# Optimization experiments

Measured on AMD Instinct MI355X. Metric: run time of the kernel, lower is better.

## Reference

```python
import jax, jax.numpy as jnp
import numpy as np

B, S, E, H = 2, 2048, 1024, 16
D = E // H


def setup_inputs() -> dict:
    key = jax.random.key(0)
    ks = jax.random.split(key, 12)
    init = lambda k, shp: (jax.random.normal(k, shp, dtype=jnp.float32) * 0.02)
    return {
        "q": jax.random.normal(ks[0], (B, S, E), dtype=jnp.float32),
        "k": jax.random.normal(ks[1], (B, S, E), dtype=jnp.float32),
        "v": jax.random.normal(ks[2], (B, S, E), dtype=jnp.float32),
        "wq": init(ks[3], (E, E)), "bq": jnp.zeros((E,), jnp.float32),
        "wk": init(ks[4], (E, E)), "bk": jnp.zeros((E,), jnp.float32),
        "wv": init(ks[5], (E, E)), "bv": jnp.zeros((E,), jnp.float32),
        "wo": init(ks[6], (E, E)), "bo": jnp.zeros((E,), jnp.float32),
        "gamma": jnp.ones((E,), jnp.float32),
        "beta": jnp.zeros((E,), jnp.float32),
        "mask": 1,
    }


def _split_heads(x):
    # [B,S,E] -> [B,H,S,D]
    return x.reshape(x.shape[0], x.shape[1], H, D).transpose(0, 2, 1, 3)


def _mha(q, k, v, wq, bq, wk, bk, wv, bv, wo, bo, gamma, beta, causal):
    residual = q
    query = _split_heads(q @ wq + bq)
    key = _split_heads(k @ wk + bk)
    value = _split_heads(v @ wv + bv)
    scale = jnp.sqrt(jnp.float32(D)) + 1e-8  # matches torch: sqrt(dk) + 1e-8
    score = jnp.einsum("bhqd,bhkd->bhqk", query, key) / scale
    if causal:
        cm = jnp.tril(jnp.ones((S, S), dtype=bool))  # 1 - triu(...,1)
        score = jnp.where(cm[None, None], score, -jnp.inf)
    attn = jax.nn.softmax(score, axis=-1)
    ctx = jnp.einsum("bhqk,bhkd->bhqd", attn, value)
    ctx = ctx.transpose(0, 2, 1, 3).reshape(ctx.shape[0], S, E)
    o = ctx @ wo + bo  # dropout is identity in eval mode
    x = residual + o
    mu = jnp.mean(x, axis=-1, keepdims=True)
    var = jnp.var(x, axis=-1, keepdims=True)
    return (x - mu) / jnp.sqrt(var + 1e-5) * gamma + beta


def reference(q, k, v, wq, bq, wk, bk, wv, bv, wo, bo, gamma, beta, mask):
    return _mha(q, k, v, wq, bq, wk, bk, wv, bv, wo, bo, gamma, beta, bool(mask))
```

## Files before the change

### kernel.cpp

```cpp
#include <hip/hip_runtime.h>
#include <hip/hip_bf16.h>

typedef __bf16 bf16x8 __attribute__((ext_vector_type(8)));
typedef __attribute__((ext_vector_type(8))) short short8_t;
typedef __attribute__((ext_vector_type(4))) short short4_t;
typedef __attribute__((ext_vector_type(4))) float f32x4;

#define DEV __device__ __forceinline__

constexpr int Bc = 2, Sc = 2048, Ec = 1024, Hc = 16, Dc = 64;
constexpr int Mc = Bc * Sc;
constexpr int NT = Sc / 64;
constexpr float kQS = (float)((1.0 / (8.0 + 1e-8)) * 1.4426950408889634);

DEV short f2bf(float f) {
  unsigned int u = __builtin_bit_cast(unsigned int, f);
  unsigned int r = u + 0x7fffu + ((u >> 16) & 1u);
  return (short)(r >> 16);
}
DEV short bfc(float f) { __bf16 h = (__bf16)f; return __builtin_bit_cast(short, h); }

DEV float fexp2(float x) {
#if __has_builtin(__builtin_amdgcn_exp2f)
  return __builtin_amdgcn_exp2f(x);
#else
  float r;
  asm("v_exp_f32 %0, %1" : "=v"(r) : "v"(x));
  return r;
#endif
}

DEV void gload16(const short* g, short* lds) {
  __builtin_amdgcn_global_load_lds((const __attribute__((address_space(1))) void*)g,
                                   (__attribute__((address_space(3))) void*)lds, 16, 0, 0);
}

struct Prep {
  const float* w[4]; short* wt[4];
  const float* x[3]; short* y[3];
};
__global__ __launch_bounds__(256) void k_prep(Prep a) {
  const int bid = blockIdx.x;
  if (bid < 4096) {
    __shared__ float tile[32][33];
    const int z = bid >> 10, bk = (bid >> 5) & 31, bn = bid & 31;
    const float* w = a.w[z];
    short* wt = a.wt[z];
    int tx = threadIdx.x & 31, ty = threadIdx.x >> 5;
#pragma unroll
    for (int i = 0; i < 4; i++)
      tile[ty + i * 8][tx] = w[(size_t)(bk * 32 + ty + i * 8) * Ec + bn * 32 + tx];
    __syncthreads();
#pragma unroll
    for (int i = 0; i < 4; i++)
      wt[(size_t)(bn * 32 + ty + i * 8) * Ec + bk * 32 + tx] = f2bf(tile[tx][ty + i * 8]);
  } else {
    const int idx = bid - 4096;
    const int z = idx >> 11, c = idx & 2047;
    const float* x = a.x[z];
    short* y = a.y[z];
    size_t i = ((size_t)c * 256 + threadIdx.x) * 8;
    float4 v0 = *(const float4*)(x + i);
    float4 v1 = *(const float4*)(x + i + 4);
    short8_t h;
    h[0] = bfc(v0.x); h[1] = bfc(v0.y); h[2] = bfc(v0.z); h[3] = bfc(v0.w);
    h[4] = bfc(v1.x); h[5] = bfc(v1.y); h[6] = bfc(v1.z); h[7] = bfc(v1.w);
    *(short8_t*)(y + i) = h;
  }
}

DEV void gemm_mfma(const short* lA, const short* lB, f32x4 (&acc)[4][4], int lane, int wm, int wn) {
#pragma unroll
  for (int kc = 0; kc < 2; kc++) {
    bf16x8 a[4], b[4];
#pragma unroll
    for (int mf = 0; mf < 4; mf++) {
      int row = wm * 64 + mf * 16 + (lane & 15);
      int ch = (kc * 4 + (lane >> 4)) ^ (row & 7);
      a[mf] = *(const bf16x8*)&lA[row * 64 + (ch << 3)];
    }
#pragma unroll
    for (int nf = 0; nf < 4; nf++) {
      int row = wn * 64 + nf * 16 + (lane & 15);
      int ch = (kc * 4 + (lane >> 4)) ^ (row & 7);
      b[nf] = *(const bf16x8*)&lB[row * 64 + (ch << 3)];
    }
#pragma unroll
    for (int mf = 0; mf < 4; mf++)
#pragma unroll
      for (int nf = 0; nf < 4; nf++)
        acc[mf][nf] = __builtin_amdgcn_mfma_f32_16x16x32_bf16(a[mf], b[nf], acc[mf][nf], 0, 0, 0);
  }
}

struct QKV3 { const short* A[3]; const short* Bt[3]; const float* bias[3]; short* out[3]; };

__global__ __launch_bounds__(256, 2) void k_gemm_qkv(QKV3 args) {
  __shared__ short lA[2][128 * 64];
  __shared__ short lB[2][128 * 64];
  int lin = blockIdx.x + 8 * blockIdx.y + 256 * blockIdx.z;
  lin = (lin & 7) * 96 + (lin >> 3);
  const int bx = lin & 7, by = (lin >> 3) & 31, z = lin >> 8;
  const short* A = args.A[z];
  const short* Bt = args.Bt[z];
  const float* bias = args.bias[z];
  short* out = args.out[z];
  const int t = threadIdx.x;
  const int m0 = by * 128, n0 = bx * 128;
  const int lane = t & 63, wid = t >> 6;
  const int wm = wid >> 1, wn = wid & 1;
  const int rl = lane >> 3, chs = ((lane & 7) ^ rl) << 3;

  f32x4 acc[4][4];
#pragma unroll
  for (int i = 0; i < 4; i++)
#pragma unroll
    for (int j = 0; j < 4; j++) acc[i][j] = {0.f, 0.f, 0.f, 0.f};

  auto stage = [&](int st, int buf) {
    const int k0 = st * 64;
#pragma unroll
    for (int j = 0; j < 4; j++) {
      int r0 = wid * 32 + j * 8;
      gload16(A + (size_t)(m0 + r0 + rl) * Ec + k0 + chs, &lA[buf][r0 * 64]);
      gload16(Bt + (size_t)(n0 + r0 + rl) * Ec + k0 + chs, &lB[buf][r0 * 64]);
    }
  };
  stage(0, 0);
  stage(1, 1);
  for (int s = 0; s < 15; s++) {
    asm volatile("s_waitcnt vmcnt(8)" ::: "memory");
    __builtin_amdgcn_s_barrier();
    gemm_mfma(lA[s & 1], lB[s & 1], acc, lane, wm, wn);
    __builtin_amdgcn_s_barrier();
    if (s + 2 < 16) stage(s + 2, s & 1);
  }
  asm volatile("s_waitcnt vmcnt(0)" ::: "memory");
  __builtin_amdgcn_s_barrier();
  gemm_mfma(lA[1], lB[1], acc, lane, wm, wn);

#pragma unroll
  for (int mf = 0; mf < 4; mf++) {
#pragma unroll
    for (int nf = 0; nf < 4; nf++) {
      int col = n0 + wn * 64 + nf * 16 + (lane & 15);
      float bs = bias[col];
      int row0 = m0 + wm * 64 + mf * 16 + ((lane >> 4) << 2);
      int bh = ((row0 >> 11) << 4) + (col >> 6);
      int d = col & 63;
      size_t bhbase = (size_t)bh * Sc * Dc;
      if (z == 0) {
#pragma unroll
        for (int r = 0; r < 4; r++) {
          int row = row0 + r;
          size_t off = bhbase + (size_t)(row & 2047) * Dc + d;
          out[off] = f2bf((acc[mf][nf][r] + bs) * kQS);
        }
      } else if (z == 1) {
#pragma unroll
        for (int r = 0; r < 4; r++) {
          int sr = (row0 + r) & 2047;
          size_t off = bhbase + (size_t)(sr >> 4) * 1024 + ((d >> 5) * 512) +
                       (((d >> 3) & 3) * 128) + ((sr & 15) * 8) + (d & 7);
          out[off] = f2bf(acc[mf][nf][r] + bs);
        }
      } else {
        short4_t h;
#pragma unroll
        for (int r = 0; r < 4; r++) h[r] = f2bf(acc[mf][nf][r] + bs);
        int s0 = row0 & 2047;
        size_t off = bhbase + (size_t)(s0 >> 6) * 4096 + (((s0 >> 5) & 1) * 2048) +
                     (((d >> 4) & 3) * 512) + ((((s0 >> 3) & 3) * 16 + (d & 15)) * 8) + (s0 & 7);
        *(short4_t*)&out[off] = h;
      }
    }
  }
}

__global__ __launch_bounds__(256, 2) void k_gemm_o(const short* __restrict__ A,
                                                   const short* __restrict__ Bt,
                                                   const float* __restrict__ bias,
                                                   const float* __restrict__ res,
                                                   float* __restrict__ out) {
  __shared__ short lA[2][128 * 64];
  __shared__ short lB[2][128 * 64];
  int lin = blockIdx.x + 8 * blockIdx.y;
  lin = (lin & 7) * 32 + (lin >> 3);
  const int bx = lin & 7, by = lin >> 3;
  const int t = threadIdx.x;
  const int m0 = by * 128, n0 = bx * 128;
  const int lane = t & 63, wid = t >> 6;
  const int wm = wid >> 1, wn = wid & 1;
  const int rl = lane >> 3, chs = ((lane & 7) ^ rl) << 3;

  f32x4 acc[4][4];
#pragma unroll
  for (int i = 0; i < 4; i++)
#pragma unroll
    for (int j = 0; j < 4; j++) acc[i][j] = {0.f, 0.f, 0.f, 0.f};

  auto stage = [&](int st, int buf) {
    const int k0 = st * 64;
#pragma unroll
    for (int j = 0; j < 4; j++) {
      int r0 = wid * 32 + j * 8;
      gload16(A + (size_t)(m0 + r0 + rl) * Ec + k0 + chs, &lA[buf][r0 * 64]);
      gload16(Bt + (size_t)(n0 + r0 + rl) * Ec + k0 + chs, &lB[buf][r0 * 64]);
    }
  };
  stage(0, 0);
  stage(1, 1);
  for (int s = 0; s < 15; s++) {
    asm volatile("s_waitcnt vmcnt(8)" ::: "memory");
    __builtin_amdgcn_s_barrier();
    gemm_mfma(lA[s & 1], lB[s & 1], acc, lane, wm, wn);
    __builtin_amdgcn_s_barrier();
    if (s + 2 < 16) stage(s + 2, s & 1);
  }
  asm volatile("s_waitcnt vmcnt(0)" ::: "memory");
  __builtin_amdgcn_s_barrier();
  gemm_mfma(lA[1], lB[1], acc, lane, wm, wn);

#pragma unroll
  for (int mf = 0; mf < 4; mf++) {
#pragma unroll
    for (int nf = 0; nf < 4; nf++) {
      int col = n0 + wn * 64 + nf * 16 + (lane & 15);
      float bs = bias[col];
#pragma unroll
      for (int r = 0; r < 4; r++) {
        int row = m0 + wm * 64 + mf * 16 + ((lane >> 4) << 2) + r;
        out[(size_t)row * Ec + col] = acc[mf][nf][r] + bs + res[(size_t)row * Ec + col];
      }
    }
  }
}

__global__ __launch_bounds__(256, 2) void k_attn8(const short* __restrict__ Qp,
                                                  const short* __restrict__ Kf,
                                                  const short* __restrict__ Vf,
                                                  const int* __restrict__ maskp,
                                                  short* __restrict__ ctx) {
  __shared__ short lP[64 * 64];
  const int lin = blockIdx.x;
  const int bh = lin & 31, qi = lin >> 5;
  const int qtA = qi, qtB = NT - 1 - qi;
  const int t = threadIdx.x, lane = t & 63, w = t >> 6;
  const int gs = lane >> 4, l15 = lane & 15;
  const bool causal = maskp[0] != 0;
  const int b = bh >> 4, h = bh & 15;
  const size_t base = (size_t)bh * Sc * Dc;
  const int ktend = causal ? qtB : (NT - 1);

  bf16x8 aqA[2], aqB[2];
  {
    const short* qpA = Qp + base + (size_t)(qtA * 64 + w * 16 + l15) * Dc + gs * 8;
    const short* qpB = Qp + base + (size_t)(qtB * 64 + w * 16 + l15) * Dc + gs * 8;
    aqA[0] = *(const bf16x8*)(qpA);
    aqA[1] = *(const bf16x8*)(qpA + 32);
    aqB[0] = *(const bf16x8*)(qpB);
    aqB[1] = *(const bf16x8*)(qpB + 32);
  }
  bf16x8 ones;
#pragma unroll
  for (int j = 0; j < 8; j++) ones[j] = (__bf16)1.0f;

  f32x4 oA[4], oB[4], lsA, lsB;
#pragma unroll
  for (int i = 0; i < 4; i++) {
    oA[i] = {0.f, 0.f, 0.f, 0.f};
    oB[i] = {0.f, 0.f, 0.f, 0.f};
  }
  lsA = {0.f, 0.f, 0.f, 0.f};
  lsB = {0.f, 0.f, 0.f, 0.f};

  const int prow = w * 16 + l15, pswz = l15 & 7;
  short* pw[4];
  const short* pr[2];
#pragma unroll
  for (int mf = 0; mf < 4; mf++)
    pw[mf] = &lP[prow * 64 + (((2 * mf + (gs >> 1)) ^ pswz) << 3) + (gs & 1) * 4];
#pragma unroll
  for (int kc = 0; kc < 2; kc++)
    pr[kc] = &lP[prow * 64 + (((kc * 4 + gs) ^ pswz) << 3)];

  const short* Kb = Kf + base + lane * 8;
  const short* Vb = Vf + base + lane * 8;
  const int qloc = w * 16 + l15;

  bf16x8 kA[2][4], kB[2][4];
#pragma unroll
  for (int mf = 0; mf < 4; mf++) {
    kA[0][mf] = *(const bf16x8*)(Kb + mf * 1024);
    kA[1][mf] = *(const bf16x8*)(Kb + mf * 1024 + 512);
  }

  int kt = 0;
  auto tilepass = [&](const bf16x8 (&kc_)[2][4], const bf16x8 (&vf)[2][4],
                      const bf16x8 (&aq)[2], f32x4 (&oacc)[4], f32x4& lsum, bool diag) {
    f32x4 s[4];
#pragma unroll
    for (int mf = 0; mf < 4; mf++) s[mf] = {0.f, 0.f, 0.f, 0.f};
    __builtin_amdgcn_s_setprio(1);
#pragma unroll
    for (int c2 = 0; c2 < 2; c2++)
#pragma unroll
      for (int mf = 0; mf < 4; mf++)
        s[mf] = __builtin_amdgcn_mfma_f32_16x16x32_bf16(kc_[c2][mf], aq[c2], s[mf], 0, 0, 0);
    __builtin_amdgcn_s_setprio(0);
    if (diag) {
#pragma unroll
      for (int mf = 0; mf < 4; mf++) {
        short4_t hh;
#pragma unroll
        for (int r = 0; r < 4; r++) {
          float p = fexp2(s[mf][r]);
          if ((mf * 16 + gs * 4 + r) > qloc) p = 0.f;
          hh[r] = bfc(p);
        }
        *(short4_t*)pw[mf] = hh;
      }
    } else {
#pragma unroll
      for (int mf = 0; mf < 4; mf++) {
        short4_t hh;
#pragma unroll
        for (int r = 0; r < 4; r++) hh[r] = bfc(fexp2(s[mf][r]));
        *(short4_t*)pw[mf] = hh;
      }
    }
    bf16x8 pa[2];
    pa[0] = *(const bf16x8*)pr[0];
    pa[1] = *(const bf16x8*)pr[1];
    __builtin_amdgcn_s_setprio(1);
#pragma unroll
    for (int c2 = 0; c2 < 2; c2++) {
      lsum = __builtin_amdgcn_mfma_f32_16x16x32_bf16(pa[c2], ones, lsum, 0, 0, 0);
#pragma unroll
      for (int df = 0; df < 4; df++)
        oacc[df] = __builtin_amdgcn_mfma_f32_16x16x32_bf16(pa[c2], vf[c2][df], oacc[df], 0, 0, 0);
    }
    __builtin_amdgcn_s_setprio(0);
  };

  auto body = [&](bf16x8 (&kc_)[2][4], bf16x8 (&kn_)[2][4]) {
    if (kt < ktend) {
      const short* kp = Kb + (kt + 1) * 4096;
#pragma unroll
      for (int mf = 0; mf < 4; mf++) {
        kn_[0][mf] = *(const bf16x8*)(kp + mf * 1024);
        kn_[1][mf] = *(const bf16x8*)(kp + mf * 1024 + 512);
      }
    }
    const short* vp = Vb + kt * 4096;
    bf16x8 vf[2][4];
#pragma unroll
    for (int c2 = 0; c2 < 2; c2++)
#pragma unroll
      for (int df = 0; df < 4; df++)
        vf[c2][df] = *(const bf16x8*)(vp + c2 * 2048 + df * 512);
    __builtin_amdgcn_sched_barrier(0);

    tilepass(kc_, vf, aqB, oB, lsB, causal && (kt == qtB));
    if (!causal || (kt <= qtA))
      tilepass(kc_, vf, aqA, oA, lsA, causal && (kt == qtA));
  };

  while (true) {
    body(kA, kB);
    if (++kt > ktend) break;
    body(kB, kA);
    if (++kt > ktend) break;
  }

#pragma unroll
  for (int r = 0; r < 4; r++) {
    float ibB = 1.0f / lsB[r];
    float ibA = 1.0f / lsA[r];
    int srB = qtB * 64 + w * 16 + (gs << 2) + r;
    int srA = qtA * 64 + w * 16 + (gs << 2) + r;
#pragma unroll
    for (int df = 0; df < 4; df++) {
      int col = h * 64 + df * 16 + l15;
      ctx[(size_t)(b * Sc + srB) * Ec + col] = f2bf(oB[df][r] * ibB);
      ctx[(size_t)(b * Sc + srA) * Ec + col] = f2bf(oA[df][r] * ibA);
    }
  }
}

__global__ __launch_bounds__(256) void k_ln(float* __restrict__ x,
                                            const float* __restrict__ gamma,
                                            const float* __restrict__ beta) {
  int row = blockIdx.x, t = threadIdx.x;
  float4 v = *(const float4*)(x + (size_t)row * Ec + t * 4);
  float s = v.x + v.y + v.z + v.w;
  float sq = v.x * v.x + v.y * v.y + v.z * v.z + v.w * v.w;
#pragma unroll
  for (int m = 1; m < 64; m <<= 1) {
    s += __shfl_xor(s, m);
    sq += __shfl_xor(sq, m);
  }
  __shared__ float red[8];
  if ((t & 63) == 0) {
    red[t >> 6] = s;
    red[4 + (t >> 6)] = sq;
  }
  __syncthreads();
  s = red[0] + red[1] + red[2] + red[3];
  sq = red[4] + red[5] + red[6] + red[7];
  float mu = s * (1.f / Ec);
  float var = sq * (1.f / Ec) - mu * mu;
  float rstd = rsqrtf(var + 1e-5f);
  float4 g = *(const float4*)(gamma + t * 4);
  float4 bb = *(const float4*)(beta + t * 4);
  v.x = (v.x - mu) * rstd * g.x + bb.x;
  v.y = (v.y - mu) * rstd * g.y + bb.y;
  v.z = (v.z - mu) * rstd * g.z + bb.z;
  v.w = (v.w - mu) * rstd * g.w + bb.w;
  *(float4*)(x + (size_t)row * Ec + t * 4) = v;
}

extern "C" void kernel_launch(void* const* d_in, const int* in_sizes, int n_in,
                              void* d_out, int out_size, void* d_ws, size_t ws_size,
                              hipStream_t stream) {
  const float* q = (const float*)d_in[0];
  const float* k = (const float*)d_in[1];
  const float* v = (const float*)d_in[2];
  const float* wq = (const float*)d_in[3];
  const float* bq = (const float*)d_in[4];
  const float* wk = (const float*)d_in[5];
  const float* bk = (const float*)d_in[6];
  const float* wv = (const float*)d_in[7];
  const float* bv = (const float*)d_in[8];
  const float* wo = (const float*)d_in[9];
  const float* bo = (const float*)d_in[10];
  const float* gamma = (const float*)d_in[11];
  const float* beta = (const float*)d_in[12];
  const int* maskp = (const int*)d_in[13];
  float* out = (float*)d_out;

  short* wtq = (short*)d_ws;
  short* wtk = wtq + (size_t)Ec * Ec;
  short* wtv = wtk + (size_t)Ec * Ec;
  short* wto = wtv + (size_t)Ec * Ec;
  short* Qp = wto + (size_t)Ec * Ec;
  short* Kf = Qp + (size_t)Mc * Ec;
  short* Vf = Kf + (size_t)Mc * Ec;
  short* ctx = Vf + (size_t)Mc * Ec;

  short* xq = (short*)d_out;
  short* xk = xq + (size_t)Mc * Ec;
  short* xv = ctx;

  dim3 tb(256);

  Prep pargs;
  pargs.w[0] = wq; pargs.w[1] = wk; pargs.w[2] = wv; pargs.w[3] = wo;
  pargs.wt[0] = wtq; pargs.wt[1] = wtk; pargs.wt[2] = wtv; pargs.wt[3] = wto;
  pargs.x[0] = q; pargs.x[1] = k; pargs.x[2] = v;
  pargs.y[0] = xq; pargs.y[1] = xk; pargs.y[2] = xv;
  k_prep<<<dim3(4096 + 3 * (Mc * Ec / 2048)), tb, 0, stream>>>(pargs);

  QKV3 gargs;
  gargs.A[0] = xq; gargs.A[1] = xk; gargs.A[2] = xv;
  gargs.Bt[0] = wtq; gargs.Bt[1] = wtk; gargs.Bt[2] = wtv;
  gargs.bias[0] = bq; gargs.bias[1] = bk; gargs.bias[2] = bv;
  gargs.out[0] = Qp; gargs.out[1] = Kf; gargs.out[2] = Vf;
  k_gemm_qkv<<<dim3(Ec / 128, Mc / 128, 3), tb, 0, stream>>>(gargs);

  k_attn8<<<dim3(NT / 2 * Bc * Hc), tb, 0, stream>>>(Qp, Kf, Vf, maskp, ctx);

  k_gemm_o<<<dim3(Ec / 128, Mc / 128), tb, 0, stream>>>(ctx, wto, bo, q, out);

  k_ln<<<dim3(Mc), tb, 0, stream>>>(out, gamma, beta);
}
```

Measured before the change: 116.3 us.

## Pre-swizzle QKV activations into MFMA fragment order and load A directly to registers

The prep kernel now writes the bf16-converted q/k/v activations in a tiled layout that matches the per-lane MFMA A-fragment order. The QKV GEMM then loads A fragments straight from global memory into registers with double buffering, instead of staging them through LDS. This halves LDS use and lets the launch bounds allow 3 blocks per CU. The cost is more register pressure, from two A register buffers, and a prep pass with strided reads.

```diff
diff --git a/kernel.cpp b/kernel.cpp
--- a/kernel.cpp
+++ b/kernel.cpp
@@ -56,16 +56,26 @@
       wt[(size_t)(bn * 32 + ty + i * 8) * Ec + bk * 32 + tx] = f2bf(tile[tx][ty + i * 8]);
   } else {
     const int idx = bid - 4096;
-    const int z = idx >> 11, c = idx & 2047;
+    const int z = idx >> 9, r = idx & 511;
+    const int mt = r >> 4, st = r & 15;
     const float* x = a.x[z];
     short* y = a.y[z];
-    size_t i = ((size_t)c * 256 + threadIdx.x) * 8;
-    float4 v0 = *(const float4*)(x + i);
-    float4 v1 = *(const float4*)(x + i + 4);
-    short8_t h;
-    h[0] = bfc(v0.x); h[1] = bfc(v0.y); h[2] = bfc(v0.z); h[3] = bfc(v0.w);
-    h[4] = bfc(v1.x); h[5] = bfc(v1.y); h[6] = bfc(v1.z); h[7] = bfc(v1.w);
-    *(short8_t*)(y + i) = h;
+    const int t = threadIdx.x;
+    const int wm = t >> 7, sf = (t >> 4) & 7, v = t & 15;
+    const int mf = sf >> 1, kc = sf & 1, gs = v >> 2, l15b = (v & 3) * 4;
+    const int k0 = st * 64 + kc * 32 + gs * 8;
+    const int row0 = mt * 128 + wm * 64 + mf * 16 + l15b;
+    short* yp = y + (size_t)mt * 131072 + st * 8192 + t * 32;
+#pragma unroll
+    for (int rr = 0; rr < 4; rr++) {
+      const float* xp = x + (size_t)(row0 + rr) * Ec + k0;
+      float4 v0 = *(const float4*)(xp);
+      float4 v1 = *(const float4*)(xp + 4);
+      short8_t h;
+      h[0] = bfc(v0.x); h[1] = bfc(v0.y); h[2] = bfc(v0.z); h[3] = bfc(v0.w);
+      h[4] = bfc(v1.x); h[5] = bfc(v1.y); h[6] = bfc(v1.z); h[7] = bfc(v1.w);
+      *(short8_t*)(yp + rr * 8) = h;
+    }
   }
 }
 
@@ -95,8 +105,7 @@
 
 struct QKV3 { const short* A[3]; const short* Bt[3]; const float* bias[3]; short* out[3]; };
 
-__global__ __launch_bounds__(256, 2) void k_gemm_qkv(QKV3 args) {
-  __shared__ short lA[2][128 * 64];
+__global__ __launch_bounds__(256, 3) void k_gemm_qkv(QKV3 args) {
   __shared__ short lB[2][128 * 64];
   int lin = blockIdx.x + 8 * blockIdx.y + 256 * blockIdx.z;
   lin = (lin & 7) * 96 + (lin >> 3);
@@ -110,6 +119,7 @@
   const int lane = t & 63, wid = t >> 6;
   const int wm = wid >> 1, wn = wid & 1;
   const int rl = lane >> 3, chs = ((lane & 7) ^ rl) << 3;
+  const short* Aw = A + (size_t)by * 131072 + wm * 4096 + lane * 8;
 
   f32x4 acc[4][4];
 #pragma unroll
@@ -117,27 +127,65 @@
 #pragma unroll
     for (int j = 0; j < 4; j++) acc[i][j] = {0.f, 0.f, 0.f, 0.f};
 
-  auto stage = [&](int st, int buf) {
+  bf16x8 rAa[2][4], rAb[2][4];
+
+  auto loadAreg = [&](int st, bf16x8 (&rc)[2][4]) {
+    const short* ap = Aw + st * 8192;
+#pragma unroll
+    for (int mf = 0; mf < 4; mf++)
+#pragma unroll
+      for (int kc = 0; kc < 2; kc++)
+        rc[kc][mf] = *(const bf16x8*)(ap + (mf * 2 + kc) * 512);
+  };
+  auto stageB = [&](int st, int buf) {
     const int k0 = st * 64;
 #pragma unroll
     for (int j = 0; j < 4; j++) {
       int r0 = wid * 32 + j * 8;
-      gload16(A + (size_t)(m0 + r0 + rl) * Ec + k0 + chs, &lA[buf][r0 * 64]);
       gload16(Bt + (size_t)(n0 + r0 + rl) * Ec + k0 + chs, &lB[buf][r0 * 64]);
     }
   };
-  stage(0, 0);
-  stage(1, 1);
-  for (int s = 0; s < 15; s++) {
-    asm volatile("s_waitcnt vmcnt(8)" ::: "memory");
+  auto mfma_frag = [&](bf16x8 (&ra)[2][4], const short* lBb) {
+#pragma unroll
+    for (int kc = 0; kc < 2; kc++) {
+      bf16x8 b[4];
+#pragma unroll
+      for (int nf = 0; nf < 4; nf++) {
+        int row = wn * 64 + nf * 16 + (lane & 15);
+        int ch = (kc * 4 + (lane >> 4)) ^ (row & 7);
+        b[nf] = *(const bf16x8*)&lBb[row * 64 + (ch << 3)];
+      }
+#pragma unroll
+      for (int mf = 0; mf < 4; mf++)
+#pragma unroll
+        for (int nf = 0; nf < 4; nf++)
+          acc[mf][nf] = __builtin_amdgcn_mfma_f32_16x16x32_bf16(ra[kc][mf], b[nf], acc[mf][nf], 0, 0, 0);
+    }
+  };
+  auto qiter = [&](int s, bf16x8 (&rc)[2][4], bool doNext) {
+    asm volatile("s_waitcnt vmcnt(12)" ::: "memory");
     __builtin_amdgcn_s_barrier();
-    gemm_mfma(lA[s & 1], lB[s & 1], acc, lane, wm, wn);
+    mfma_frag(rc, lB[s & 1]);
+    if (doNext) loadAreg(s + 2, rc);
     __builtin_amdgcn_s_barrier();
-    if (s + 2 < 16) stage(s + 2, s & 1);
-  }
+    if (doNext) stageB(s + 2, s & 1);
+  };
+
+  loadAreg(0, rAa);
+  stageB(0, 0);
+  stageB(1, 1);
+  loadAreg(1, rAb);
+
+  for (int s = 0; s < 12; s += 2) {
+    qiter(s, rAa, true);
+    qiter(s + 1, rAb, true);
+  }
+  qiter(12, rAa, true);
+  qiter(13, rAb, true);
+  qiter(14, rAa, false);
   asm volatile("s_waitcnt vmcnt(0)" ::: "memory");
   __builtin_amdgcn_s_barrier();
-  gemm_mfma(lA[1], lB[1], acc, lane, wm, wn);
+  mfma_frag(rAb, lB[1]);
 
 #pragma unroll
   for (int mf = 0; mf < 4; mf++) {
@@ -459,7 +507,7 @@
   pargs.wt[0] = wtq; pargs.wt[1] = wtk; pargs.wt[2] = wtv; pargs.wt[3] = wto;
   pargs.x[0] = q; pargs.x[1] = k; pargs.x[2] = v;
   pargs.y[0] = xq; pargs.y[1] = xk; pargs.y[2] = xv;
-  k_prep<<<dim3(4096 + 3 * (Mc * Ec / 2048)), tb, 0, stream>>>(pargs);
+  k_prep<<<dim3(4096 + 3 * 512), tb, 0, stream>>>(pargs);
 
   QKV3 gargs;
   gargs.A[0] = xq; gargs.A[1] = xk; gargs.A[2] = xv;
```

Result: slower. 125.3 us (+7.7%).

## Enlarge QKV GEMM tile to 256x256 with 512-thread blocks

Applied to the files above, without the earlier changes.

The fused QKV projection GEMM moves from 128x128 tiles with 4 waves to 256x256 tiles with 8 waves, launched as a flat grid of 192 blocks with a remapped swizzle. Each wave now computes a 128x64 sub-tile from double-buffered LDS halves, with operand loads interleaved per quarter. The aim is higher arithmetic intensity per global byte and fewer redundant loads of A and B. In exchange the grid has fewer blocks than the CU count, and LDS use per block is much larger, which limits occupancy.

```diff
diff --git a/kernel.cpp b/kernel.cpp
--- a/kernel.cpp
+++ b/kernel.cpp
@@ -95,57 +95,106 @@
 
 struct QKV3 { const short* A[3]; const short* Bt[3]; const float* bias[3]; short* out[3]; };
 
-__global__ __launch_bounds__(256, 2) void k_gemm_qkv(QKV3 args) {
-  __shared__ short lA[2][128 * 64];
-  __shared__ short lB[2][128 * 64];
-  int lin = blockIdx.x + 8 * blockIdx.y + 256 * blockIdx.z;
-  lin = (lin & 7) * 96 + (lin >> 3);
-  const int bx = lin & 7, by = (lin >> 3) & 31, z = lin >> 8;
+__global__ __launch_bounds__(512, 2) void k_gemm_qkv(QKV3 args) {
+  __shared__ short lA[2][2][128 * 64];
+  __shared__ short lB[2][2][128 * 64];
+  int lin = blockIdx.x;
+  lin = (lin & 7) * 24 + (lin >> 3);
+  const int bx = lin & 3, by = (lin >> 2) & 15, z = lin >> 6;
   const short* A = args.A[z];
   const short* Bt = args.Bt[z];
   const float* bias = args.bias[z];
   short* out = args.out[z];
   const int t = threadIdx.x;
-  const int m0 = by * 128, n0 = bx * 128;
+  const int m0 = by * 256, n0 = bx * 256;
   const int lane = t & 63, wid = t >> 6;
-  const int wm = wid >> 1, wn = wid & 1;
+  const int wr = wid >> 2, wc = wid & 3;
+  const int gs = lane >> 4, l15 = lane & 15;
   const int rl = lane >> 3, chs = ((lane & 7) ^ rl) << 3;
 
-  f32x4 acc[4][4];
-#pragma unroll
-  for (int i = 0; i < 4; i++)
+  f32x4 acc[8][4];
+#pragma unroll
+  for (int i = 0; i < 8; i++)
 #pragma unroll
     for (int j = 0; j < 4; j++) acc[i][j] = {0.f, 0.f, 0.f, 0.f};
 
-  auto stage = [&](int st, int buf) {
+  auto stage4 = [&](int st, int buf) {
     const int k0 = st * 64;
 #pragma unroll
-    for (int j = 0; j < 4; j++) {
-      int r0 = wid * 32 + j * 8;
-      gload16(A + (size_t)(m0 + r0 + rl) * Ec + k0 + chs, &lA[buf][r0 * 64]);
-      gload16(Bt + (size_t)(n0 + r0 + rl) * Ec + k0 + chs, &lB[buf][r0 * 64]);
+    for (int half = 0; half < 2; half++) {
+#pragma unroll
+      for (int j = 0; j < 2; j++) {
+        int r0 = wid * 16 + j * 8;
+        gload16(A + (size_t)(m0 + half * 128 + r0 + rl) * Ec + k0 + chs, &lA[buf][half][r0 * 64]);
+      }
+    }
+#pragma unroll
+    for (int half = 0; half < 2; half++) {
+#pragma unroll
+      for (int j = 0; j < 2; j++) {
+        int r0 = wid * 16 + j * 8;
+        gload16(Bt + (size_t)(n0 + half * 128 + r0 + rl) * Ec + k0 + chs, &lB[buf][half][r0 * 64]);
+      }
     }
   };
-  stage(0, 0);
-  stage(1, 1);
+
+  auto compute = [&](int buf) {
+    const short* hA = lA[buf][wr];
+    const short* hB = lB[buf][wc >> 1];
+    const int nsub = (wc & 1) * 64;
+#pragma unroll
+    for (int qm = 0; qm < 2; qm++) {
+#pragma unroll
+      for (int qn = 0; qn < 2; qn++) {
+        bf16x8 a[2][4], b[2][2];
+#pragma unroll
+        for (int kc = 0; kc < 2; kc++)
+#pragma unroll
+          for (int m2 = 0; m2 < 4; m2++) {
+            int row = qm * 64 + m2 * 16 + l15;
+            int ch = (kc * 4 + gs) ^ (row & 7);
+            a[kc][m2] = *(const bf16x8*)&hA[row * 64 + (ch << 3)];
+          }
+#pragma unroll
+        for (int kc = 0; kc < 2; kc++)
+#pragma unroll
+          for (int n2 = 0; n2 < 2; n2++) {
+            int row = nsub + qn * 32 + n2 * 16 + l15;
+            int ch = (kc * 4 + gs) ^ (row & 7);
+            b[kc][n2] = *(const bf16x8*)&hB[row * 64 + (ch << 3)];
+          }
+#pragma unroll
+        for (int kc = 0; kc < 2; kc++)
+#pragma unroll
+          for (int m2 = 0; m2 < 4; m2++)
+#pragma unroll
+            for (int n2 = 0; n2 < 2; n2++)
+              acc[qm * 4 + m2][qn * 2 + n2] = __builtin_amdgcn_mfma_f32_16x16x32_bf16(
+                  a[kc][m2], b[kc][n2], acc[qm * 4 + m2][qn * 2 + n2], 0, 0, 0);
+      }
+    }
+  };
+
+  stage4(0, 0);
+  stage4(1, 1);
   for (int s = 0; s < 15; s++) {
     asm volatile("s_waitcnt vmcnt(8)" ::: "memory");
     __builtin_amdgcn_s_barrier();
-    gemm_mfma(lA[s & 1], lB[s & 1], acc, lane, wm, wn);
+    compute(s & 1);
     __builtin_amdgcn_s_barrier();
-    if (s + 2 < 16) stage(s + 2, s & 1);
+    if (s + 2 < 16) stage4(s + 2, s & 1);
   }
   asm volatile("s_waitcnt vmcnt(0)" ::: "memory");
   __builtin_amdgcn_s_barrier();
-  gemm_mfma(lA[1], lB[1], acc, lane, wm, wn);
-
-#pragma unroll
-  for (int mf = 0; mf < 4; mf++) {
+  compute(1);
+
+#pragma unroll
+  for (int mf = 0; mf < 8; mf++) {
 #pragma unroll
     for (int nf = 0; nf < 4; nf++) {
-      int col = n0 + wn * 64 + nf * 16 + (lane & 15);
+      int col = n0 + wc * 64 + nf * 16 + l15;
       float bs = bias[col];
-      int row0 = m0 + wm * 64 + mf * 16 + ((lane >> 4) << 2);
+      int row0 = m0 + wr * 128 + mf * 16 + (gs << 2);
       int bh = ((row0 >> 11) << 4) + (col >> 6);
       int d = col & 63;
       size_t bhbase = (size_t)bh * Sc * Dc;
@@ -466,7 +515,7 @@
   gargs.Bt[0] = wtq; gargs.Bt[1] = wtk; gargs.Bt[2] = wtv;
   gargs.bias[0] = bq; gargs.bias[1] = bk; gargs.bias[2] = bv;
   gargs.out[0] = Qp; gargs.out[1] = Kf; gargs.out[2] = Vf;
-  k_gemm_qkv<<<dim3(Ec / 128, Mc / 128, 3), tb, 0, stream>>>(gargs);
+  k_gemm_qkv<<<dim3(192), dim3(512), 0, stream>>>(gargs);
 
   k_attn8<<<dim3(NT / 2 * Bc * Hc), tb, 0, stream>>>(Qp, Kf, Vf, maskp, ctx);
 
```

Result: no change. 115.2 us (-1.0%).

## Enlarge QKV GEMM tiles to 256x256 with 512 threads and 4-stage pipeline

Applied to the files above, without the earlier changes.

Reworks the fused QKV projection GEMM to use 256x256 output tiles per 512-thread block, with a K-step of 32 and a four-buffer LDS ring that keeps three stages in flight. This raises arithmetic intensity per global load and drops one barrier per iteration by issuing the next stage before the compute. In exchange there are fewer blocks (192 total, which may underfill the GPU's CUs) and higher register pressure from 32 accumulators per thread.

```diff
diff --git a/kernel.cpp b/kernel.cpp
--- a/kernel.cpp
+++ b/kernel.cpp
@@ -95,57 +95,85 @@
 
 struct QKV3 { const short* A[3]; const short* Bt[3]; const float* bias[3]; short* out[3]; };
 
-__global__ __launch_bounds__(256, 2) void k_gemm_qkv(QKV3 args) {
-  __shared__ short lA[2][128 * 64];
-  __shared__ short lB[2][128 * 64];
-  int lin = blockIdx.x + 8 * blockIdx.y + 256 * blockIdx.z;
-  lin = (lin & 7) * 96 + (lin >> 3);
-  const int bx = lin & 7, by = (lin >> 3) & 31, z = lin >> 8;
+__global__ __launch_bounds__(512, 2) void k_gemm_qkv(QKV3 args) {
+  __shared__ short lA[4][256 * 32];
+  __shared__ short lB[4][256 * 32];
+  int lin = blockIdx.x;
+  lin = (lin & 7) * 24 + (lin >> 3);
+  const int bx = lin & 3, by = (lin >> 2) & 15, z = lin >> 6;
   const short* A = args.A[z];
   const short* Bt = args.Bt[z];
   const float* bias = args.bias[z];
   short* out = args.out[z];
   const int t = threadIdx.x;
-  const int m0 = by * 128, n0 = bx * 128;
+  const int m0 = by * 256, n0 = bx * 256;
   const int lane = t & 63, wid = t >> 6;
-  const int wm = wid >> 1, wn = wid & 1;
-  const int rl = lane >> 3, chs = ((lane & 7) ^ rl) << 3;
-
-  f32x4 acc[4][4];
-#pragma unroll
-  for (int i = 0; i < 4; i++)
+  const int wr = wid >> 2, wc = wid & 3;
+  const int gs = lane >> 4, l15 = lane & 15;
+
+  const int slot0 = wid * 128 + lane;
+  const int row_a = slot0 >> 2, ch_a = slot0 & 3;
+  const int slot1 = slot0 + 64;
+  const int row_b = slot1 >> 2, ch_b = slot1 & 3;
+
+  f32x4 acc[8][4];
+#pragma unroll
+  for (int i = 0; i < 8; i++)
 #pragma unroll
     for (int j = 0; j < 4; j++) acc[i][j] = {0.f, 0.f, 0.f, 0.f};
 
   auto stage = [&](int st, int buf) {
-    const int k0 = st * 64;
-#pragma unroll
-    for (int j = 0; j < 4; j++) {
-      int r0 = wid * 32 + j * 8;
-      gload16(A + (size_t)(m0 + r0 + rl) * Ec + k0 + chs, &lA[buf][r0 * 64]);
-      gload16(Bt + (size_t)(n0 + r0 + rl) * Ec + k0 + chs, &lB[buf][r0 * 64]);
-    }
+    const int k0 = st * 32;
+    gload16(A + (size_t)(m0 + row_a) * Ec + k0 + ((ch_a ^ (row_a & 3)) << 3), &lA[buf][(wid * 128) * 8]);
+    gload16(A + (size_t)(m0 + row_b) * Ec + k0 + ((ch_b ^ (row_b & 3)) << 3), &lA[buf][(wid * 128 + 64) * 8]);
+    gload16(Bt + (size_t)(n0 + row_a) * Ec + k0 + ((ch_a ^ (row_a & 3)) << 3), &lB[buf][(wid * 128) * 8]);
+    gload16(Bt + (size_t)(n0 + row_b) * Ec + k0 + ((ch_b ^ (row_b & 3)) << 3), &lB[buf][(wid * 128 + 64) * 8]);
   };
+
+  auto compute = [&](int buf) {
+    bf16x8 a[8], b[4];
+#pragma unroll
+    for (int m2 = 0; m2 < 8; m2++) {
+      int row = wr * 128 + m2 * 16 + l15;
+      int ch = gs ^ (row & 3);
+      a[m2] = *(const bf16x8*)&lA[buf][row * 32 + (ch << 3)];
+    }
+#pragma unroll
+    for (int n2 = 0; n2 < 4; n2++) {
+      int row = wc * 64 + n2 * 16 + l15;
+      int ch = gs ^ (row & 3);
+      b[n2] = *(const bf16x8*)&lB[buf][row * 32 + (ch << 3)];
+    }
+#pragma unroll
+    for (int m2 = 0; m2 < 8; m2++)
+#pragma unroll
+      for (int n2 = 0; n2 < 4; n2++)
+        acc[m2][n2] = __builtin_amdgcn_mfma_f32_16x16x32_bf16(a[m2], b[n2], acc[m2][n2], 0, 0, 0);
+  };
+
   stage(0, 0);
   stage(1, 1);
-  for (int s = 0; s < 15; s++) {
+  stage(2, 2);
+  for (int s = 0; s < 30; s++) {
     asm volatile("s_waitcnt vmcnt(8)" ::: "memory");
     __builtin_amdgcn_s_barrier();
-    gemm_mfma(lA[s & 1], lB[s & 1], acc, lane, wm, wn);
-    __builtin_amdgcn_s_barrier();
-    if (s + 2 < 16) stage(s + 2, s & 1);
-  }
+    if (s + 3 < 32) stage(s + 3, (s + 3) & 3);
+    compute(s & 3);
+  }
+  asm volatile("s_waitcnt vmcnt(4)" ::: "memory");
+  __builtin_amdgcn_s_barrier();
+  compute(30 & 3);
   asm volatile("s_waitcnt vmcnt(0)" ::: "memory");
   __builtin_amdgcn_s_barrier();
-  gemm_mfma(lA[1], lB[1], acc, lane, wm, wn);
-
-#pragma unroll
-  for (int mf = 0; mf < 4; mf++) {
+  compute(31 & 3);
+
+#pragma unroll
+  for (int mf = 0; mf < 8; mf++) {
 #pragma unroll
     for (int nf = 0; nf < 4; nf++) {
-      int col = n0 + wn * 64 + nf * 16 + (lane & 15);
+      int col = n0 + wc * 64 + nf * 16 + l15;
       float bs = bias[col];
-      int row0 = m0 + wm * 64 + mf * 16 + ((lane >> 4) << 2);
+      int row0 = m0 + wr * 128 + mf * 16 + (gs << 2);
       int bh = ((row0 >> 11) << 4) + (col >> 6);
       int d = col & 63;
       size_t bhbase = (size_t)bh * Sc * Dc;
@@ -466,7 +494,7 @@
   gargs.Bt[0] = wtq; gargs.Bt[1] = wtk; gargs.Bt[2] = wtv;
   gargs.bias[0] = bq; gargs.bias[1] = bk; gargs.bias[2] = bv;
   gargs.out[0] = Qp; gargs.out[1] = Kf; gargs.out[2] = Vf;
-  k_gemm_qkv<<<dim3(Ec / 128, Mc / 128, 3), tb, 0, stream>>>(gargs);
+  k_gemm_qkv<<<dim3(192), dim3(512), 0, stream>>>(gargs);
 
   k_attn8<<<dim3(NT / 2 * Bc * Hc), tb, 0, stream>>>(Qp, Kf, Vf, maskp, ctx);
 
```

Result: slower. 129.5 us (+11.3%).
